# Kernel tuning notes

Measured on AMD Instinct MI355X. Metric: run time of the kernel, lower is better.

## Reference

```python
import jax, jax.numpy as jnp
import numpy as np

B, F, D = 4096, 32, 32
LAYER_SIZE = [128, 128]


def setup_inputs() -> dict:
    key = jax.random.key(0)
    k1, k2, k3 = jax.random.split(key, 3)
    inputs = jax.random.normal(k1, (B, F, D), dtype=jnp.float32)
    # CIN filters: shape [1, field_nums[0]*field_nums[i], field_nums[i+1]]
    field_nums = [F] + LAYER_SIZE
    filter_0 = (jax.random.normal(k2, (1, field_nums[0] * field_nums[0], field_nums[1]), dtype=jnp.float32) * 0.05)
    filter_1 = (jax.random.normal(k3, (1, field_nums[0] * field_nums[1], field_nums[2]), dtype=jnp.float32) * 0.05)
    return {"inputs": inputs, "filter_0": filter_0, "filter_1": filter_1}


def _cin_forward(inputs, filters):
    x0 = inputs          # [B, F, D] -- hidden_nn_layers[0]
    prev = inputs        # hidden_nn_layers[-1]
    outs = []
    for W in filters:    # W: [1, F*M, N]
        # outer product over field dims: [B, F, M, D]
        z = jnp.einsum('bhd,bmd->bhmd', x0, prev)
        b, h, m, d = z.shape
        z = z.reshape(b, h * m, d)                 # [B, F*M, D]
        # 1x1 conv over the F*M axis == contraction with W[0]: [F*M, N]
        cur = jnp.einsum('bpd,pn->bnd', z, W[0])   # [B, N, D]
        cur = jax.nn.relu(cur)
        prev = cur
        outs.append(cur)
    result = jnp.concatenate(outs, axis=1)         # [B, sum(layer_size), D]
    return jnp.sum(result, axis=-1)                # [B, sum(layer_size)]


def reference(inputs, filter_0, filter_1):
    return _cin_forward(inputs, (filter_0, filter_1))
```

## Files before the change

### kernel.cpp

```cpp
#include <hip/hip_runtime.h>


typedef _Float16 half_t;
typedef _Float16 half4v __attribute__((ext_vector_type(4)));
typedef _Float16 half8 __attribute__((ext_vector_type(8)));
typedef float f32x16 __attribute__((ext_vector_type(16)));

template <int M>
__global__ void prep_w_kernel(const float* __restrict__ W,
                              half_t* __restrict__ Wp) {
  int gid = blockIdx.x * 256 + threadIdx.x;
  int n = gid & 127;
  int r = gid >> 7;
  int t = r & 15;
  int s = r >> 4;
  int h = s & 31;
  int mc = s >> 5;
  int k = h * M + mc * 16 + t;
  Wp[(((s * 2 + (t >> 3)) * 128 + n) << 3) + (t & 7)] = (half_t)W[k * 128 + n];
}

__global__ __launch_bounds__(256, 4) void cin_fused_kernel(
    const float* __restrict__ x0,
    const half_t* __restrict__ Wp0,
    const half_t* __restrict__ Wp1,
    float* __restrict__ out) {
  __shared__ half_t xsf[4 * 32 * 32];
  __shared__ half_t prevT[4 * 32 * 128];
  half_t* xT = prevT;

  const int tid = threadIdx.x;
  const int b0 = blockIdx.x * 4;

  const float4* x4 = (const float4*)(x0 + (size_t)b0 * 1024);
#pragma unroll
  for (int r = 0; r < 4; ++r) {
    int q = r * 256 + tid;
    float4 v = x4[q];
    int e = q * 4;
    int bi = e >> 10, h = (e >> 5) & 31, d0 = e & 31;
    half4v hv = {(half_t)v.x, (half_t)v.y, (half_t)v.z, (half_t)v.w};
    *(half4v*)&xsf[(bi * 32 + h) * 32 + d0] = hv;
    xT[(bi * 32 + d0 + 0) * 40 + h] = hv[0];
    xT[(bi * 32 + d0 + 1) * 40 + h] = hv[1];
    xT[(bi * 32 + d0 + 2) * 40 + h] = hv[2];
    xT[(bi * 32 + d0 + 3) * 40 + h] = hv[3];
  }
  __syncthreads();

  const int lane = tid & 63;
  const int l31 = lane & 31;
  const int hi = lane >> 5;
  const int wave = tid >> 6;
  const int n0 = wave * 32;

  const f32x16 z16 = {0.f, 0.f, 0.f, 0.f, 0.f, 0.f, 0.f, 0.f,
                      0.f, 0.f, 0.f, 0.f, 0.f, 0.f, 0.f, 0.f};
  f32x16 acc[4];
#pragma unroll
  for (int rt = 0; rt < 4; ++rt) acc[rt] = z16;

  const half_t* wp0 = Wp0 + (size_t)hi * 1024 + (size_t)(n0 + l31) * 8;
  const half_t* wp1 = Wp1 + (size_t)hi * 1024 + (size_t)(n0 + l31) * 8;

#pragma unroll 1
  for (int mc = 0; mc < 2; ++mc) {
    half8 P[4];
#pragma unroll
    for (int rt = 0; rt < 4; ++rt)
      P[rt] = *(const half8*)&xT[(rt * 32 + l31) * 40 + mc * 16 + hi * 8];
    const half_t* wrow = wp0 + (size_t)mc * 32 * 2048;
#pragma unroll 2
    for (int h = 0; h < 32; ++h) {
      half8 Bf = *(const half8*)(wrow + (size_t)h * 2048);
#pragma unroll
      for (int rt = 0; rt < 4; ++rt) {
        half_t xv = xsf[(rt * 32 + h) * 32 + l31];
        half8 Af = P[rt] * xv;
        acc[rt] = __builtin_amdgcn_mfma_f32_32x32x16_f16(Af, Bf, acc[rt], 0, 0, 0);
      }
    }
  }

  __syncthreads();

#pragma unroll
  for (int rt = 0; rt < 4; ++rt) {
    float s = 0.f;
#pragma unroll
    for (int r = 0; r < 16; ++r) {
      float v = acc[rt][r];
      v = v > 0.f ? v : 0.f;
      s += v;
      int d = (r & 3) + ((r >> 2) * 8) + hi * 4;
      prevT[(rt * 32 + d) * 128 + n0 + l31] = (half_t)v;
    }
    s += __shfl_down(s, 32);
    if (lane < 32) out[(size_t)(b0 + rt) * 256 + n0 + lane] = s;
    acc[rt] = z16;
  }
  __syncthreads();

#pragma unroll 1
  for (int mc = 0; mc < 8; ++mc) {
    half8 P[4];
#pragma unroll
    for (int rt = 0; rt < 4; ++rt)
      P[rt] = *(const half8*)&prevT[(rt * 32 + l31) * 128 + mc * 16 + hi * 8];
    const half_t* wrow = wp1 + (size_t)mc * 32 * 2048;
#pragma unroll 2
    for (int h = 0; h < 32; ++h) {
      half8 Bf = *(const half8*)(wrow + (size_t)h * 2048);
#pragma unroll
      for (int rt = 0; rt < 4; ++rt) {
        half_t xv = xsf[(rt * 32 + h) * 32 + l31];
        half8 Af = P[rt] * xv;
        acc[rt] = __builtin_amdgcn_mfma_f32_32x32x16_f16(Af, Bf, acc[rt], 0, 0, 0);
      }
    }
  }

#pragma unroll
  for (int rt = 0; rt < 4; ++rt) {
    float s = 0.f;
#pragma unroll
    for (int r = 0; r < 16; ++r) {
      float v = acc[rt][r];
      s += v > 0.f ? v : 0.f;
    }
    s += __shfl_down(s, 32);
    if (lane < 32)
      out[(size_t)(b0 + rt) * 256 + 128 + n0 + lane] = s;
  }
}

extern "C" void kernel_launch(void* const* d_in, const int* in_sizes, int n_in,
                              void* d_out, int out_size, void* d_ws,
                              size_t ws_size, hipStream_t stream) {
  const float* x0 = (const float*)d_in[0];
  const float* w0 = (const float*)d_in[1];
  const float* w1 = (const float*)d_in[2];
  float* out = (float*)d_out;
  char* ws = (char*)d_ws;

  half_t* Wp0 = (half_t*)(ws);
  half_t* Wp1 = (half_t*)(ws + 64 * 2048 * 2);

  hipLaunchKernelGGL((prep_w_kernel<32>), dim3(512), dim3(256), 0, stream, w0,
                     Wp0);
  hipLaunchKernelGGL((prep_w_kernel<128>), dim3(2048), dim3(256), 0, stream,
                     w1, Wp1);
  hipLaunchKernelGGL(cin_fused_kernel, dim3(1024), dim3(256), 0, stream, x0,
                     Wp0, Wp1, out);
}
```

Baseline: 217.0 us.

## Prefetch weight fragments, interleave x across batch, swizzle prevT, merge prep kernels

Merges the two weight-prep launches into one kernel that writes 8-wide half vectors. In the main kernel the x operand is stored batch-interleaved, so one half4 LDS load supplies the scale for all four row tiles. Weight fragments for the next two h steps are loaded from global memory one iteration ahead, hiding latency behind the MFMAs. prevT gets an XOR swizzle to cut LDS bank conflicts. The prefetching adds register pressure under the 4-waves launch bound, and the strided column writes in xsf2 may themselves conflict.

```diff
diff --git a/kernel.cpp b/kernel.cpp
--- a/kernel.cpp
+++ b/kernel.cpp
@@ -6,18 +6,29 @@
 typedef _Float16 half8 __attribute__((ext_vector_type(8)));
 typedef float f32x16 __attribute__((ext_vector_type(16)));
 
-template <int M>
-__global__ void prep_w_kernel(const float* __restrict__ W,
-                              half_t* __restrict__ Wp) {
+__global__ void prep_w_kernel(const float* __restrict__ W0,
+                              const float* __restrict__ W1,
+                              half_t* __restrict__ Wp0,
+                              half_t* __restrict__ Wp1) {
   int gid = blockIdx.x * 256 + threadIdx.x;
   int n = gid & 127;
-  int r = gid >> 7;
-  int t = r & 15;
-  int s = r >> 4;
-  int h = s & 31;
-  int mc = s >> 5;
-  int k = h * M + mc * 16 + t;
-  Wp[(((s * 2 + (t >> 3)) * 128 + n) << 3) + (t & 7)] = (half_t)W[k * 128 + n];
+  int tg = (gid >> 7) & 1;
+  int s = gid >> 8;
+  const float* W;
+  half_t* Wp;
+  int M, sl;
+  if (s < 64) { W = W0; Wp = Wp0; M = 32; sl = s; }
+  else        { W = W1; Wp = Wp1; M = 128; sl = s - 64; }
+  int h = sl & 31, mc = sl >> 5;
+  int kbase = h * M + mc * 16 + tg * 8;
+  half8 v;
+#pragma unroll
+  for (int j = 0; j < 8; ++j) v[j] = (half_t)W[(size_t)(kbase + j) * 128 + n];
+  *(half8*)(Wp + ((size_t)(sl * 2 + tg) * 128 + n) * 8) = v;
+}
+
+__device__ __forceinline__ int pswz(int row, int m) {
+  return row * 128 + ((((m) >> 3) ^ (row & 15)) << 3) + (m & 7);
 }
 
 __global__ __launch_bounds__(256, 4) void cin_fused_kernel(
@@ -25,7 +36,7 @@
     const half_t* __restrict__ Wp0,
     const half_t* __restrict__ Wp1,
     float* __restrict__ out) {
-  __shared__ half_t xsf[4 * 32 * 32];
+  __shared__ half_t xsf2[32 * 32 * 4];
   __shared__ half_t prevT[4 * 32 * 128];
   half_t* xT = prevT;
 
@@ -40,11 +51,11 @@
     int e = q * 4;
     int bi = e >> 10, h = (e >> 5) & 31, d0 = e & 31;
     half4v hv = {(half_t)v.x, (half_t)v.y, (half_t)v.z, (half_t)v.w};
-    *(half4v*)&xsf[(bi * 32 + h) * 32 + d0] = hv;
-    xT[(bi * 32 + d0 + 0) * 40 + h] = hv[0];
-    xT[(bi * 32 + d0 + 1) * 40 + h] = hv[1];
-    xT[(bi * 32 + d0 + 2) * 40 + h] = hv[2];
-    xT[(bi * 32 + d0 + 3) * 40 + h] = hv[3];
+#pragma unroll
+    for (int j = 0; j < 4; ++j) {
+      xsf2[(h * 32 + d0 + j) * 4 + bi] = hv[j];
+      xT[(bi * 32 + d0 + j) * 40 + h] = hv[j];
+    }
   }
   __syncthreads();
 
@@ -54,31 +65,45 @@
   const int wave = tid >> 6;
   const int n0 = wave * 32;
 
-  const f32x16 z16 = {0.f, 0.f, 0.f, 0.f, 0.f, 0.f, 0.f, 0.f,
-                      0.f, 0.f, 0.f, 0.f, 0.f, 0.f, 0.f, 0.f};
   f32x16 acc[4];
 #pragma unroll
-  for (int rt = 0; rt < 4; ++rt) acc[rt] = z16;
+  for (int rt = 0; rt < 4; ++rt)
+#pragma unroll
+    for (int r = 0; r < 16; ++r) acc[rt][r] = 0.f;
 
-  const half_t* wp0 = Wp0 + (size_t)hi * 1024 + (size_t)(n0 + l31) * 8;
-  const half_t* wp1 = Wp1 + (size_t)hi * 1024 + (size_t)(n0 + l31) * 8;
+  const int woff = hi * 1024 + (n0 + l31) * 8;
+  const half_t* xrd = &xsf2[l31 * 4];
 
+  half8 P[4];
+  half8 Bc0, Bc1;
+
+  Bc0 = *(const half8*)(Wp0 + 0 * 2048 + woff);
+  Bc1 = *(const half8*)(Wp0 + 1 * 2048 + woff);
 #pragma unroll 1
   for (int mc = 0; mc < 2; ++mc) {
-    half8 P[4];
 #pragma unroll
     for (int rt = 0; rt < 4; ++rt)
       P[rt] = *(const half8*)&xT[(rt * 32 + l31) * 40 + mc * 16 + hi * 8];
-    const half_t* wrow = wp0 + (size_t)mc * 32 * 2048;
-#pragma unroll 2
-    for (int h = 0; h < 32; ++h) {
-      half8 Bf = *(const half8*)(wrow + (size_t)h * 2048);
+#pragma unroll 1
+    for (int gg = 0; gg < 16; ++gg) {
+      int s2 = mc * 32 + gg * 2;
+      int sn = (s2 + 2) & 63;
+      half8 Bn0 = *(const half8*)(Wp0 + (size_t)sn * 2048 + woff);
+      half8 Bn1 = *(const half8*)(Wp0 + (size_t)(sn + 1) * 2048 + woff);
 #pragma unroll
-      for (int rt = 0; rt < 4; ++rt) {
-        half_t xv = xsf[(rt * 32 + h) * 32 + l31];
-        half8 Af = P[rt] * xv;
-        acc[rt] = __builtin_amdgcn_mfma_f32_32x32x16_f16(Af, Bf, acc[rt], 0, 0, 0);
+      for (int j = 0; j < 2; ++j) {
+        int h = gg * 2 + j;
+        half4v xq = *(const half4v*)(xrd + h * 128);
+        half8 B = j ? Bc1 : Bc0;
+#pragma unroll
+        for (int rt = 0; rt < 4; ++rt) {
+          half8 Af = P[rt] * xq[rt];
+          acc[rt] =
+              __builtin_amdgcn_mfma_f32_32x32x16_f16(Af, B, acc[rt], 0, 0, 0);
+        }
       }
+      Bc0 = Bn0;
+      Bc1 = Bn1;
     }
   }
 
@@ -92,31 +117,42 @@
       float v = acc[rt][r];
       v = v > 0.f ? v : 0.f;
       s += v;
-      int d = (r & 3) + ((r >> 2) * 8) + hi * 4;
-      prevT[(rt * 32 + d) * 128 + n0 + l31] = (half_t)v;
+      int d = (r & 3) + ((r >> 2) << 3) + hi * 4;
+      prevT[pswz(rt * 32 + d, n0 + l31)] = (half_t)v;
+      acc[rt][r] = 0.f;
     }
     s += __shfl_down(s, 32);
     if (lane < 32) out[(size_t)(b0 + rt) * 256 + n0 + lane] = s;
-    acc[rt] = z16;
   }
   __syncthreads();
 
+  Bc0 = *(const half8*)(Wp1 + 0 * 2048 + woff);
+  Bc1 = *(const half8*)(Wp1 + 1 * 2048 + woff);
 #pragma unroll 1
   for (int mc = 0; mc < 8; ++mc) {
-    half8 P[4];
 #pragma unroll
     for (int rt = 0; rt < 4; ++rt)
-      P[rt] = *(const half8*)&prevT[(rt * 32 + l31) * 128 + mc * 16 + hi * 8];
-    const half_t* wrow = wp1 + (size_t)mc * 32 * 2048;
-#pragma unroll 2
-    for (int h = 0; h < 32; ++h) {
-      half8 Bf = *(const half8*)(wrow + (size_t)h * 2048);
+      P[rt] = *(const half8*)&prevT[pswz(rt * 32 + l31, mc * 16 + hi * 8)];
+#pragma unroll 1
+    for (int gg = 0; gg < 16; ++gg) {
+      int s2 = mc * 32 + gg * 2;
+      int sn = (s2 + 2) & 255;
+      half8 Bn0 = *(const half8*)(Wp1 + (size_t)sn * 2048 + woff);
+      half8 Bn1 = *(const half8*)(Wp1 + (size_t)(sn + 1) * 2048 + woff);
 #pragma unroll
-      for (int rt = 0; rt < 4; ++rt) {
-        half_t xv = xsf[(rt * 32 + h) * 32 + l31];
-        half8 Af = P[rt] * xv;
-        acc[rt] = __builtin_amdgcn_mfma_f32_32x32x16_f16(Af, Bf, acc[rt], 0, 0, 0);
+      for (int j = 0; j < 2; ++j) {
+        int h = gg * 2 + j;
+        half4v xq = *(const half4v*)(xrd + h * 128);
+        half8 B = j ? Bc1 : Bc0;
+#pragma unroll
+        for (int rt = 0; rt < 4; ++rt) {
+          half8 Af = P[rt] * xq[rt];
+          acc[rt] =
+              __builtin_amdgcn_mfma_f32_32x32x16_f16(Af, B, acc[rt], 0, 0, 0);
+        }
       }
+      Bc0 = Bn0;
+      Bc1 = Bn1;
     }
   }
 
@@ -129,8 +165,7 @@
       s += v > 0.f ? v : 0.f;
     }
     s += __shfl_down(s, 32);
-    if (lane < 32)
-      out[(size_t)(b0 + rt) * 256 + 128 + n0 + lane] = s;
+    if (lane < 32) out[(size_t)(b0 + rt) * 256 + 128 + n0 + lane] = s;
   }
 }
 
@@ -146,10 +181,8 @@
   half_t* Wp0 = (half_t*)(ws);
   half_t* Wp1 = (half_t*)(ws + 64 * 2048 * 2);
 
-  hipLaunchKernelGGL((prep_w_kernel<32>), dim3(512), dim3(256), 0, stream, w0,
-                     Wp0);
-  hipLaunchKernelGGL((prep_w_kernel<128>), dim3(2048), dim3(256), 0, stream,
-                     w1, Wp1);
+  hipLaunchKernelGGL(prep_w_kernel, dim3(320), dim3(256), 0, stream, w0, w1,
+                     Wp0, Wp1);
   hipLaunchKernelGGL(cin_fused_kernel, dim3(1024), dim3(256), 0, stream, x0,
                      Wp0, Wp1, out);
 }
```

Measured after the change: 215.3 us. No clear change (-0.8%).
